# Kernel optimization log

Measured on AMD Instinct MI355X. Metric: run time of the kernel, lower is better.

## Reference

```python
import jax, jax.numpy as jnp
import numpy as np


def sinusoidal_pe(d, length, dtype=jnp.float32):
    """Standard transformer sin/cos positional encoding along the W axis.
    Returns (d, length): pe[2i, p] = sin(p/10000^(2i/d)), pe[2i+1, p] = cos(...)."""
    pos = jnp.arange(length, dtype=dtype)[None, :]            # (1, W)
    i = jnp.arange(0, d, 2, dtype=dtype)[:, None]             # (d//2, 1)
    div = jnp.exp(-i * (np.log(10000.0) / d))                 # (d//2, 1)
    ang = pos * div                                           # (d//2, W)
    pe = jnp.zeros((d, length), dtype)
    pe = pe.at[0::2].set(jnp.sin(ang)).at[1::2].set(jnp.cos(ang))
    return pe


def setup_inputs() -> dict:
    key = jax.random.key(0)
    ks = jax.random.split(key, 8)
    B, C, D, H, W = 2, 64, 32, 64, 96
    q_k_dim = 32
    s = 1.0 / np.sqrt(C)
    return {
        "x": jax.random.normal(ks[0], (B, C, D, H, W), jnp.float32),
        "Wq": jax.random.normal(ks[1], (q_k_dim, C), jnp.float32) * s,
        "bq": jax.random.normal(ks[2], (q_k_dim,), jnp.float32) * 0.01,
        "Wk": jax.random.normal(ks[3], (q_k_dim, C), jnp.float32) * s,
        "bk": jax.random.normal(ks[4], (q_k_dim,), jnp.float32) * 0.01,
        "Wv": jax.random.normal(ks[5], (C, C), jnp.float32) * s,
        "bv": jax.random.normal(ks[6], (C,), jnp.float32) * 0.01,
        "gamma": jax.random.normal(ks[7], (1,), jnp.float32) * 0.1,
    }


def reference(x, Wq, bq, Wk, bk, Wv, bv, gamma):
    # x: (B, C, D, H, W)
    B, C, D, H, W = x.shape
    qk = Wq.shape[0]
    # 1x1x1 Conv3d == per-voxel channel matmul
    Q = jnp.einsum('bcdhw,qc->bqdhw', x, Wq) + bq[None, :, None, None, None]
    K = jnp.einsum('bcdhw,qc->bqdhw', x, Wk) + bk[None, :, None, None, None]
    V = jnp.einsum('bcdhw,vc->bvdhw', x, Wv) + bv[None, :, None, None, None]
    # additive sinusoidal positional encoding along the row (W) axis
    pe_qk = sinusoidal_pe(qk, W, x.dtype)[None, :, None, None, :]
    pe_v = sinusoidal_pe(C, W, x.dtype)[None, :, None, None, :]
    Q = Q + pe_qk
    K = K + pe_qk
    V = V + pe_v
    # row attention: scores over the W axis, independently per (b, d, h)
    # attn[b,d,h,i,j] = sum_q Q[b,q,d,h,i] * K[b,q,d,h,j]  (no 1/sqrt(d) scaling, as in source)
    attn = jax.nn.softmax(jnp.einsum('bqdhi,bqdhj->bdhij', Q, K), axis=-1)
    # out[b,c,d,h,i] = sum_j V[b,c,d,h,j] * attn[b,d,h,i,j]
    out = jnp.einsum('bcdhj,bdhij->bcdhi', V, attn)
    return gamma * out + x
```

## Files before the change

### kernel.cpp

```cpp
#include <hip/hip_runtime.h>
#include <hip/hip_bf16.h>
#include <math.h>

constexpr int Cc = 64, Dd = 32, Hh = 64, Ww = 96, QKd = 32;
constexpr int CSTRIDE = Dd * Hh * Ww;
constexpr int BDIM = 256;

#define FREQ_QK 0.28782313662425574f
#define FREQ_V  0.14391156831212787f

typedef __bf16 bf16_t;
typedef bf16_t bf16x8 __attribute__((ext_vector_type(8)));
typedef bf16_t bf16x4 __attribute__((ext_vector_type(4)));
typedef float  floatx4 __attribute__((ext_vector_type(4)));

constexpr int XS_STRIDE = 72;
constexpr int QS_STRIDE = 40;
constexpr int VS_STRIDE = 104;
constexpr int PS_STRIDE = 104;
constexpr int OFF_QS = 9984;
constexpr int OFF_KS = 9984 + 3840;
constexpr int OFF_VS = 9984 + 7680;
constexpr int SMEM_ELEMS = 9984 + 7680 + 6656;

__global__ __launch_bounds__(BDIM, 3)
void row_attn_mfma(const float* __restrict__ x,
                   const float* __restrict__ Wq, const float* __restrict__ bq,
                   const float* __restrict__ Wk, const float* __restrict__ bk,
                   const float* __restrict__ Wv, const float* __restrict__ bv,
                   const float* __restrict__ gamma,
                   float* __restrict__ y)
{
    __shared__ __align__(16) bf16_t smem[SMEM_ELEMS];
    bf16_t* Xs = smem;
    bf16_t* Ps = smem;
    bf16_t* Qs = smem + OFF_QS;
    bf16_t* Ks = smem + OFF_KS;
    bf16_t* Vs = smem + OFF_VS;

    const int t    = threadIdx.x;
    const int lane = t & 63;
    const int wid  = t >> 6;
    const int l16  = lane & 15;
    const int quad = lane >> 4;

    const int bid = blockIdx.x;
    const int b   = bid / (Dd * Hh);
    const int rem = bid % (Dd * Hh);
    const int d   = rem / Hh;
    const int h   = rem % Hh;
    const int base0 = b * (Cc * CSTRIDE) + d * (Hh * Ww) + h * Ww;

#pragma unroll
    for (int k = 0; k < 12; ++k) {
        int idx = t + k * BDIM;
        int w  = idx % Ww;
        int c  = (idx / Ww) * 2;
        float v0 = x[base0 + c * CSTRIDE + w];
        float v1 = x[base0 + (c + 1) * CSTRIDE + w];
        unsigned short u0 = __builtin_bit_cast(unsigned short, (bf16_t)v0);
        unsigned short u1 = __builtin_bit_cast(unsigned short, (bf16_t)v1);
        *(unsigned int*)(&Xs[w * XS_STRIDE + c]) = (unsigned)u0 | ((unsigned)u1 << 16);
    }

    const float* Wmat = (wid == 0) ? Wq : (wid == 1) ? Wk : Wv;
    const float* bias = (wid == 0) ? bq : (wid == 1) ? bk : bv;
    const float freqc = (wid < 2) ? FREQ_QK : FREQ_V;
    const int   mbase = (wid == 3) ? 32 : 0;

    bf16x8 wfrag[2][2];
#pragma unroll
    for (int mt = 0; mt < 2; ++mt)
#pragma unroll
        for (int kt = 0; kt < 2; ++kt) {
            const float* p = Wmat + (mbase + mt * 16 + l16) * 64 + kt * 32 + quad * 8;
            float4 lo = *(const float4*)p;
            float4 hi = *(const float4*)(p + 4);
            bf16x8 f;
            f[0] = (bf16_t)lo.x; f[1] = (bf16_t)lo.y; f[2] = (bf16_t)lo.z; f[3] = (bf16_t)lo.w;
            f[4] = (bf16_t)hi.x; f[5] = (bf16_t)hi.y; f[6] = (bf16_t)hi.z; f[7] = (bf16_t)hi.w;
            wfrag[mt][kt] = f;
        }
    float biasv[2][4], freq2[2][2];
#pragma unroll
    for (int mt = 0; mt < 2; ++mt) {
#pragma unroll
        for (int r = 0; r < 4; ++r)
            biasv[mt][r] = bias[mbase + mt * 16 + quad * 4 + r];
#pragma unroll
        for (int p2 = 0; p2 < 2; ++p2)
            freq2[mt][p2] = __expf(-(float)(mbase + mt * 16 + quad * 4 + 2 * p2) * freqc);
    }
    __syncthreads();

    bf16_t* dstQK = (wid == 0) ? Qs : Ks;
#pragma unroll
    for (int nt = 0; nt < 6; ++nt) {
        bf16x8 bfr[2];
#pragma unroll
        for (int kt = 0; kt < 2; ++kt)
            bfr[kt] = *(const bf16x8*)(&Xs[(nt * 16 + l16) * XS_STRIDE + kt * 32 + quad * 8]);
#pragma unroll
        for (int mt = 0; mt < 2; ++mt) {
            floatx4 acc = {0.f, 0.f, 0.f, 0.f};
            acc = __builtin_amdgcn_mfma_f32_16x16x32_bf16(wfrag[mt][0], bfr[0], acc, 0, 0, 0);
            acc = __builtin_amdgcn_mfma_f32_16x16x32_bf16(wfrag[mt][1], bfr[1], acc, 0, 0, 0);
            float wv = (float)(nt * 16 + l16);
            float out[4];
#pragma unroll
            for (int p2 = 0; p2 < 2; ++p2) {
                float sn, cs;
                __sincosf(wv * freq2[mt][p2], &sn, &cs);
                out[2 * p2]     = acc[2 * p2]     + biasv[mt][2 * p2]     + sn;
                out[2 * p2 + 1] = acc[2 * p2 + 1] + biasv[mt][2 * p2 + 1] + cs;
            }
            if (wid < 2) {
                bf16x4 pk;
                pk[0] = (bf16_t)out[0]; pk[1] = (bf16_t)out[1];
                pk[2] = (bf16_t)out[2]; pk[3] = (bf16_t)out[3];
                *(bf16x4*)(&dstQK[(nt * 16 + l16) * QS_STRIDE + mt * 16 + quad * 4]) = pk;
            } else {
#pragma unroll
                for (int r = 0; r < 4; ++r)
                    Vs[(mbase + mt * 16 + quad * 4 + r) * VS_STRIDE + nt * 16 + l16] = (bf16_t)out[r];
            }
        }
    }
    __syncthreads();

    const int it0 = (wid < 2) ? wid * 2 : wid + 2;
    const int itc = (wid < 2) ? 2 : 1;
    for (int ii = 0; ii < itc; ++ii) {
        const int it = it0 + ii;
        bf16x8 afr = *(const bf16x8*)(&Qs[(it * 16 + l16) * QS_STRIDE + quad * 8]);
        floatx4 sacc[6];
#pragma unroll
        for (int jt = 0; jt < 6; ++jt) {
            bf16x8 bfr = *(const bf16x8*)(&Ks[(jt * 16 + l16) * QS_STRIDE + quad * 8]);
            floatx4 z = {0.f, 0.f, 0.f, 0.f};
            sacc[jt] = __builtin_amdgcn_mfma_f32_16x16x32_bf16(afr, bfr, z, 0, 0, 0);
        }
#pragma unroll
        for (int r = 0; r < 4; ++r) {
            float m = sacc[0][r];
#pragma unroll
            for (int jt = 1; jt < 6; ++jt) m = fmaxf(m, sacc[jt][r]);
#pragma unroll
            for (int msk = 1; msk < 16; msk <<= 1) m = fmaxf(m, __shfl_xor(m, msk));
            float e[6], sum = 0.f;
#pragma unroll
            for (int jt = 0; jt < 6; ++jt) { e[jt] = __expf(sacc[jt][r] - m); sum += e[jt]; }
#pragma unroll
            for (int msk = 1; msk < 16; msk <<= 1) sum += __shfl_xor(sum, msk);
            float inv = 1.0f / sum;
            int row = it * 16 + quad * 4 + r;
#pragma unroll
            for (int jt = 0; jt < 6; ++jt)
                Ps[row * PS_STRIDE + jt * 16 + l16] = (bf16_t)(e[jt] * inv);
        }
    }
    __syncthreads();

    const float g = gamma[0];
    const int ct = wid;
    bf16x8 vfr[3];
#pragma unroll
    for (int ks = 0; ks < 3; ++ks)
        vfr[ks] = *(const bf16x8*)(&Vs[(ct * 16 + l16) * VS_STRIDE + ks * 32 + quad * 8]);
#pragma unroll
    for (int it = 0; it < 6; ++it) {
        floatx4 acc = {0.f, 0.f, 0.f, 0.f};
#pragma unroll
        for (int ks = 0; ks < 3; ++ks) {
            bf16x8 bfr = *(const bf16x8*)(&Ps[(it * 16 + l16) * PS_STRIDE + ks * 32 + quad * 8]);
            acc = __builtin_amdgcn_mfma_f32_16x16x32_bf16(vfr[ks], bfr, acc, 0, 0, 0);
        }
#pragma unroll
        for (int r = 0; r < 4; ++r) {
            int c  = ct * 16 + quad * 4 + r;
            int gi = base0 + c * CSTRIDE + it * 16 + l16;
            y[gi] = fmaf(g, acc[r], x[gi]);
        }
    }
}

extern "C" void kernel_launch(void* const* d_in, const int* in_sizes, int n_in,
                              void* d_out, int out_size, void* d_ws, size_t ws_size,
                              hipStream_t stream) {
    const float* x     = (const float*)d_in[0];
    const float* Wq    = (const float*)d_in[1];
    const float* bq    = (const float*)d_in[2];
    const float* Wk    = (const float*)d_in[3];
    const float* bk    = (const float*)d_in[4];
    const float* Wv    = (const float*)d_in[5];
    const float* bv    = (const float*)d_in[6];
    const float* gamma = (const float*)d_in[7];
    float* y = (float*)d_out;

    dim3 grid(2 * 32 * 64);
    row_attn_mfma<<<grid, BDIM, 0, stream>>>(x, Wq, bq, Wk, bk, Wv, bv, gamma, y);
}
```

Baseline: 216.1 us.

## Transpose score MFMA, swizzle Q/K LDS, shrink smem for higher occupancy

Computes scores as K·Q so each lane holds a full query row segment, which makes the softmax reductions mostly in-register with two cross-quad shuffles and lets P be written as packed bf16x4. Q is pre-scaled by log2(e) so exp2f can be used, and the reciprocal uses the hardware rcp. Q/K LDS rows drop their padding in favour of an XOR swizzle, and Q/K fragments are loaded into registers before a barrier so P can reuse the smaller shared region. Together these cut LDS use and allow four blocks per CU, at the cost of an extra barrier and possible register pressure under the tighter launch bound.

```diff
diff --git a/kernel.cpp b/kernel.cpp
--- a/kernel.cpp
+++ b/kernel.cpp
@@ -8,6 +8,7 @@
 
 #define FREQ_QK 0.28782313662425574f
 #define FREQ_V  0.14391156831212787f
+#define LOG2E   1.44269504088896340736f
 
 typedef __bf16 bf16_t;
 typedef bf16_t bf16x8 __attribute__((ext_vector_type(8)));
@@ -15,15 +16,15 @@
 typedef float  floatx4 __attribute__((ext_vector_type(4)));
 
 constexpr int XS_STRIDE = 72;
-constexpr int QS_STRIDE = 40;
+constexpr int QS_STRIDE = 32;
 constexpr int VS_STRIDE = 104;
 constexpr int PS_STRIDE = 104;
-constexpr int OFF_QS = 9984;
-constexpr int OFF_KS = 9984 + 3840;
-constexpr int OFF_VS = 9984 + 7680;
-constexpr int SMEM_ELEMS = 9984 + 7680 + 6656;
-
-__global__ __launch_bounds__(BDIM, 3)
+constexpr int OFF_QS = 6912;
+constexpr int OFF_KS = 6912 + 3072;
+constexpr int OFF_VS = OFF_KS + 3072;
+constexpr int SMEM_ELEMS = OFF_VS + 6656;
+
+__global__ __launch_bounds__(BDIM, 4)
 void row_attn_mfma(const float* __restrict__ x,
                    const float* __restrict__ Wq, const float* __restrict__ bq,
                    const float* __restrict__ Wk, const float* __restrict__ bk,
@@ -115,10 +116,16 @@
                 out[2 * p2 + 1] = acc[2 * p2 + 1] + biasv[mt][2 * p2 + 1] + cs;
             }
             if (wid < 2) {
+                if (wid == 0) {
+#pragma unroll
+                    for (int r = 0; r < 4; ++r) out[r] *= LOG2E;
+                }
                 bf16x4 pk;
                 pk[0] = (bf16_t)out[0]; pk[1] = (bf16_t)out[1];
                 pk[2] = (bf16_t)out[2]; pk[3] = (bf16_t)out[3];
-                *(bf16x4*)(&dstQK[(nt * 16 + l16) * QS_STRIDE + mt * 16 + quad * 4]) = pk;
+                const int w  = nt * 16 + l16;
+                const int el = (w * QS_STRIDE + mt * 16 + quad * 4) ^ ((w & 7) << 3);
+                *(bf16x4*)(&dstQK[el]) = pk;
             } else {
 #pragma unroll
                 for (int r = 0; r < 4; ++r)
@@ -130,33 +137,58 @@
 
     const int it0 = (wid < 2) ? wid * 2 : wid + 2;
     const int itc = (wid < 2) ? 2 : 1;
+    bf16x8 qfr[2];
+#pragma unroll
+    for (int ii = 0; ii < 2; ++ii) {
+        const int it = it0 + ((itc == 2) ? ii : 0);
+        const int w  = it * 16 + l16;
+        qfr[ii] = *(const bf16x8*)(&Qs[(w * QS_STRIDE + quad * 8) ^ ((w & 7) << 3)]);
+    }
+    bf16x8 kfr[6];
+#pragma unroll
+    for (int jt = 0; jt < 6; ++jt) {
+        const int w = jt * 16 + l16;
+        kfr[jt] = *(const bf16x8*)(&Ks[(w * QS_STRIDE + quad * 8) ^ ((w & 7) << 3)]);
+    }
+    __syncthreads();
+
     for (int ii = 0; ii < itc; ++ii) {
         const int it = it0 + ii;
-        bf16x8 afr = *(const bf16x8*)(&Qs[(it * 16 + l16) * QS_STRIDE + quad * 8]);
         floatx4 sacc[6];
 #pragma unroll
         for (int jt = 0; jt < 6; ++jt) {
-            bf16x8 bfr = *(const bf16x8*)(&Ks[(jt * 16 + l16) * QS_STRIDE + quad * 8]);
             floatx4 z = {0.f, 0.f, 0.f, 0.f};
-            sacc[jt] = __builtin_amdgcn_mfma_f32_16x16x32_bf16(afr, bfr, z, 0, 0, 0);
-        }
-#pragma unroll
-        for (int r = 0; r < 4; ++r) {
-            float m = sacc[0][r];
-#pragma unroll
-            for (int jt = 1; jt < 6; ++jt) m = fmaxf(m, sacc[jt][r]);
-#pragma unroll
-            for (int msk = 1; msk < 16; msk <<= 1) m = fmaxf(m, __shfl_xor(m, msk));
-            float e[6], sum = 0.f;
-#pragma unroll
-            for (int jt = 0; jt < 6; ++jt) { e[jt] = __expf(sacc[jt][r] - m); sum += e[jt]; }
-#pragma unroll
-            for (int msk = 1; msk < 16; msk <<= 1) sum += __shfl_xor(sum, msk);
-            float inv = 1.0f / sum;
-            int row = it * 16 + quad * 4 + r;
-#pragma unroll
-            for (int jt = 0; jt < 6; ++jt)
-                Ps[row * PS_STRIDE + jt * 16 + l16] = (bf16_t)(e[jt] * inv);
+            sacc[jt] = __builtin_amdgcn_mfma_f32_16x16x32_bf16(kfr[jt], qfr[ii], z, 0, 0, 0);
+        }
+        float mr[6];
+#pragma unroll
+        for (int jt = 0; jt < 6; ++jt)
+            mr[jt] = fmaxf(fmaxf(sacc[jt][0], sacc[jt][1]), fmaxf(sacc[jt][2], sacc[jt][3]));
+        float m = fmaxf(fmaxf(fmaxf(mr[0], mr[1]), fmaxf(mr[2], mr[3])), fmaxf(mr[4], mr[5]));
+        m = fmaxf(m, __shfl_xor(m, 16));
+        m = fmaxf(m, __shfl_xor(m, 32));
+        float sum = 0.f;
+#pragma unroll
+        for (int jt = 0; jt < 6; ++jt) {
+#pragma unroll
+            for (int r = 0; r < 4; ++r) {
+                float e = exp2f(sacc[jt][r] - m);
+                sacc[jt][r] = e;
+                sum += e;
+            }
+        }
+        sum += __shfl_xor(sum, 16);
+        sum += __shfl_xor(sum, 32);
+        const float inv = __builtin_amdgcn_rcpf(sum);
+        const int row = it * 16 + l16;
+#pragma unroll
+        for (int jt = 0; jt < 6; ++jt) {
+            bf16x4 pk;
+            pk[0] = (bf16_t)(sacc[jt][0] * inv);
+            pk[1] = (bf16_t)(sacc[jt][1] * inv);
+            pk[2] = (bf16_t)(sacc[jt][2] * inv);
+            pk[3] = (bf16_t)(sacc[jt][3] * inv);
+            *(bf16x4*)(&Ps[row * PS_STRIDE + jt * 16 + quad * 4]) = pk;
         }
     }
     __syncthreads();
```

After: 214.2 us. Within noise of the previous version (-0.9%).
